# Performance work log

Measured on AMD Instinct MI355X. Metric: run time of the kernel, lower is better.

Reference implementation:

```python
import jax, jax.numpy as jnp
import numpy as np

CHUNK = 32
PRIOR = 64
POSE = 512
PRED = 128
B = 2048


def setup_inputs() -> dict:
    key = jax.random.key(0)
    k1, k2, k3, k4, k5, k6 = jax.random.split(key, 6)
    initial_feature = jax.random.normal(k1, (B, PRIOR, POSE), dtype=jnp.float32)
    pred_feature = jax.random.normal(k2, (B, PRED, POSE), dtype=jnp.float32)
    s1 = 1.0 / np.sqrt(CHUNK * POSE)
    s2 = 1.0 / np.sqrt(POSE)
    W1 = jax.random.uniform(k3, (POSE, CHUNK * POSE), minval=-s1, maxval=s1, dtype=jnp.float32)
    b1 = jax.random.uniform(k4, (POSE,), minval=-s1, maxval=s1, dtype=jnp.float32)
    W2 = jax.random.uniform(k5, (POSE, POSE), minval=-s2, maxval=s2, dtype=jnp.float32)
    b2 = jax.random.uniform(k6, (POSE,), minval=-s2, maxval=s2, dtype=jnp.float32)
    return {"initial_feature": initial_feature, "pred_feature": pred_feature,
            "W1": W1, "b1": b1, "W2": W2, "b2": b2}


def reference(initial_feature, pred_feature, W1, b1, W2, b2):
    Bn = initial_feature.shape[0]
    # last CHUNK prior frames flattened -> [B, CHUNK*POSE]
    x = initial_feature[:, PRIOR - CHUNK:, :].reshape(Bn, -1)
    # spatial_chunk_encoder (Dropout is identity in eval mode)
    mem = (x @ W1.T + b1) @ W2.T + b2          # [B, POSE]
    head = pred_feature[:, :CHUNK, :]          # [B, CHUNK, POSE]
    score = jnp.einsum('bd,bcd->bc', mem, head)  # per-token dot product
    g = jax.nn.sigmoid(score)[..., None]       # [B, CHUNK, 1]
    blended = g * head + (1.0 - g) * mem[:, None, :]
    return pred_feature.at[:, :CHUNK, :].set(blended)
```

## Files before the change

kernel.cpp:

```cpp
#include <hip/hip_runtime.h>
#include <hip/hip_bf16.h>
#include <stdint.h>

#define CHUNKC 32
#define PRIORC 64
#define POSEC 512
#define PREDC 128
#define NB 2048
#define K1 (CHUNKC*POSEC)
#define KS 8
#define KCH (K1/KS)

typedef __attribute__((ext_vector_type(8))) short bf16x8;
typedef __attribute__((ext_vector_type(4))) float f32x4;

__device__ __forceinline__ unsigned short f2b(float f) {
    union { float f; unsigned int u; } x; x.f = f;
    unsigned int r = x.u + 0x7fffu + ((x.u >> 16) & 1u);
    return (unsigned short)(r >> 16);
}

__device__ __forceinline__ void gload_lds16(const void* g, void* l) {
    __builtin_amdgcn_global_load_lds(
        (const __attribute__((address_space(1))) unsigned int*)g,
        (__attribute__((address_space(3))) unsigned int*)l, 16, 0, 0);
}

#define XN4   8388608
#define W1N4  2097152
#define W2N4  65536
__global__ __launch_bounds__(256) void cvt_all_kernel(const float4* __restrict__ init,
                                                      const float4* __restrict__ W1,
                                                      const float4* __restrict__ W2,
                                                      ushort4* __restrict__ xb,
                                                      ushort4* __restrict__ w1b,
                                                      ushort4* __restrict__ w2b) {
    const int64_t n = XN4 + W1N4 + W2N4;
    const int64_t stride = (int64_t)gridDim.x * blockDim.x;
    for (int64_t i = (int64_t)blockIdx.x * blockDim.x + threadIdx.x; i < n; i += stride) {
        float4 v; ushort4* dst;
        if (i < XN4) {
            int64_t b = i >> 12, r = i & 4095;
            v = init[b * 8192 + 4096 + r];
            dst = xb + i;
        } else if (i < XN4 + W1N4) {
            v = W1[i - XN4];
            dst = w1b + (i - XN4);
        } else {
            v = W2[i - XN4 - W1N4];
            dst = w2b + (i - XN4 - W1N4);
        }
        *dst = make_ushort4(f2b(v.x), f2b(v.y), f2b(v.z), f2b(v.w));
    }
}

__global__ __launch_bounds__(256, 4) void gemm1_kernel(const ushort* __restrict__ xb,
                                                       const ushort* __restrict__ w1b,
                                                       float* __restrict__ part) {
    __shared__ ushort As[64][64];
    __shared__ ushort Bs[128][64];
    const int t = threadIdx.x;
    const int l = t & 63, wid = t >> 6;
    const int wr = wid >> 1, wc = wid & 1;
    const int orig = (blockIdx.x & 7) * 128 + (blockIdx.x >> 3);
    const int mt = orig & 31, nt = (orig >> 5) & 3, ks = orig >> 7;

    f32x4 acc[2][4] = {};

    const ushort* aG = xb  + (int64_t)(mt * 64)  * K1 + ks * KCH;
    const ushort* bG = w1b + (int64_t)(nt * 128) * K1 + ks * KCH;
    const int srow = t >> 3, scol = (t & 7) * 8;

    const int fr = l & 15, fq = l >> 4;

    for (int k0 = 0; k0 < KCH; k0 += 64) {
#pragma unroll
        for (int i = 0; i < 2; ++i)
            gload_lds16(aG + (int64_t)(i * 32 + srow) * K1 + k0 + scol,
                        (char*)&As[0][0] + i * 4096 + wid * 1024);
#pragma unroll
        for (int i = 0; i < 4; ++i)
            gload_lds16(bG + (int64_t)(i * 32 + srow) * K1 + k0 + scol,
                        (char*)&Bs[0][0] + i * 4096 + wid * 1024);
        __syncthreads();
#pragma unroll
        for (int k2 = 0; k2 < 2; ++k2) {
            bf16x8 a[2], b[4];
#pragma unroll
            for (int m = 0; m < 2; ++m)
                a[m] = *(const bf16x8*)&As[wr * 32 + m * 16 + fr][k2 * 32 + fq * 8];
#pragma unroll
            for (int n = 0; n < 4; ++n)
                b[n] = *(const bf16x8*)&Bs[wc * 64 + n * 16 + fr][k2 * 32 + fq * 8];
#pragma unroll
            for (int m = 0; m < 2; ++m)
#pragma unroll
                for (int n = 0; n < 4; ++n)
                    acc[m][n] = __builtin_amdgcn_mfma_f32_16x16x32_bf16(a[m], b[n], acc[m][n], 0, 0, 0);
        }
        __syncthreads();
    }

    float* P = part + (int64_t)ks * NB * POSEC;
    const int mbase = mt * 64 + wr * 32, nbase = nt * 128 + wc * 64;
#pragma unroll
    for (int m = 0; m < 2; ++m)
#pragma unroll
        for (int n = 0; n < 4; ++n) {
            int row0 = mbase + m * 16 + fq * 4;
            int col  = nbase + n * 16 + fr;
#pragma unroll
            for (int r = 0; r < 4; ++r)
                P[(int64_t)(row0 + r) * POSEC + col] = acc[m][n][r];
        }
}

__global__ __launch_bounds__(256) void reduce_kernel(const float4* __restrict__ part,
                                                     const float* __restrict__ b1,
                                                     ushort4* __restrict__ A2) {
    const int i4 = blockIdx.x * 256 + threadIdx.x;
    float4 s = part[i4];
#pragma unroll
    for (int k = 1; k < KS; ++k) {
        float4 p = part[(int64_t)k * 262144 + i4];
        s.x += p.x; s.y += p.y; s.z += p.z; s.w += p.w;
    }
    const int col = (i4 * 4) & 511;
    float4 bv = *(const float4*)&b1[col];
    A2[i4] = make_ushort4(f2b(s.x + bv.x), f2b(s.y + bv.y), f2b(s.z + bv.z), f2b(s.w + bv.w));
}

__global__ __launch_bounds__(256) void gemm2_kernel(const ushort* __restrict__ A2,
                                                    const ushort* __restrict__ w2b,
                                                    const float* __restrict__ b2,
                                                    float* __restrict__ mem) {
    __shared__ ushort As[64][64];
    __shared__ ushort Bs[64][64];
    const int t = threadIdx.x;
    const int l = t & 63, wid = t >> 6;
    const int wr = wid >> 1, wc = wid & 1;
    const int mt = blockIdx.x >> 3, nt = blockIdx.x & 7;

    f32x4 acc[2][2] = {};
    const ushort* aG = A2  + (int64_t)(mt * 64) * POSEC;
    const ushort* bG = w2b + (int64_t)(nt * 64) * POSEC;
    const int srow = t >> 3, scol = (t & 7) * 8;
    const int fr = l & 15, fq = l >> 4;

    for (int k0 = 0; k0 < POSEC; k0 += 64) {
#pragma unroll
        for (int i = 0; i < 2; ++i) {
            gload_lds16(aG + (int64_t)(i * 32 + srow) * POSEC + k0 + scol,
                        (char*)&As[0][0] + i * 4096 + wid * 1024);
            gload_lds16(bG + (int64_t)(i * 32 + srow) * POSEC + k0 + scol,
                        (char*)&Bs[0][0] + i * 4096 + wid * 1024);
        }
        __syncthreads();
#pragma unroll
        for (int k2 = 0; k2 < 2; ++k2) {
            bf16x8 a[2], b[2];
#pragma unroll
            for (int m = 0; m < 2; ++m)
                a[m] = *(const bf16x8*)&As[wr * 32 + m * 16 + fr][k2 * 32 + fq * 8];
#pragma unroll
            for (int n = 0; n < 2; ++n)
                b[n] = *(const bf16x8*)&Bs[wc * 32 + n * 16 + fr][k2 * 32 + fq * 8];
#pragma unroll
            for (int m = 0; m < 2; ++m)
#pragma unroll
                for (int n = 0; n < 2; ++n)
                    acc[m][n] = __builtin_amdgcn_mfma_f32_16x16x32_bf16(a[m], b[n], acc[m][n], 0, 0, 0);
        }
        __syncthreads();
    }

    const int mbase = mt * 64 + wr * 32, nbase = nt * 64 + wc * 32;
#pragma unroll
    for (int m = 0; m < 2; ++m)
#pragma unroll
        for (int n = 0; n < 2; ++n) {
            int row0 = mbase + m * 16 + fq * 4;
            int col  = nbase + n * 16 + fr;
            float bias = b2[col];
#pragma unroll
            for (int r = 0; r < 4; ++r)
                mem[(int64_t)(row0 + r) * POSEC + col] = acc[m][n][r] + bias;
        }
}

__global__ __launch_bounds__(256) void blend_kernel(const float* __restrict__ pred,
                                                    const float* __restrict__ mem,
                                                    float* __restrict__ out) {
    const int b = blockIdx.x;
    const int t = threadIdx.x;
    __shared__ float sm[POSEC];
    __shared__ float sg[CHUNKC];

    sm[t]       = mem[(int64_t)b * POSEC + t];
    sm[t + 256] = mem[(int64_t)b * POSEC + 256 + t];
    __syncthreads();

    const int l = t & 63, wid = t >> 6;
    const float4* sm4 = (const float4*)sm;
    const float4* p4 = (const float4*)pred + (int64_t)b * 16384;
    float4* o4 = (float4*)out + (int64_t)b * 16384;

#pragma unroll
    for (int ci = 0; ci < 8; ++ci) {
        int c = wid * 8 + ci;
        float4 h0 = p4[c * 128 + l * 2];
        float4 h1 = p4[c * 128 + l * 2 + 1];
        float4 m0 = sm4[l * 2];
        float4 m1 = sm4[l * 2 + 1];
        float s = h0.x * m0.x + h0.y * m0.y + h0.z * m0.z + h0.w * m0.w
                + h1.x * m1.x + h1.y * m1.y + h1.z * m1.z + h1.w * m1.w;
#pragma unroll
        for (int o = 32; o; o >>= 1) s += __shfl_xor(s, o);
        if (l == 0) sg[c] = 1.0f / (1.0f + expf(-s));
    }
    __syncthreads();

#pragma unroll
    for (int i = 0; i < 16; ++i) {
        int idx = i * 256 + t;
        int row = idx >> 7, c4 = idx & 127;
        float g = sg[row];
        float4 h = p4[idx];
        float4 m = sm4[c4];
        float4 r;
        r.x = g * h.x + (1.0f - g) * m.x;
        r.y = g * h.y + (1.0f - g) * m.y;
        r.z = g * h.z + (1.0f - g) * m.z;
        r.w = g * h.w + (1.0f - g) * m.w;
        o4[idx] = r;
    }
#pragma unroll
    for (int i = 0; i < 48; ++i) {
        int idx = 4096 + i * 256 + t;
        o4[idx] = p4[idx];
    }
}


extern "C" void kernel_launch(void* const* d_in, const int* in_sizes, int n_in,
                              void* d_out, int out_size, void* d_ws, size_t ws_size,
                              hipStream_t stream) {
    const float* init = (const float*)d_in[0];
    const float* pred = (const float*)d_in[1];
    const float* W1   = (const float*)d_in[2];
    const float* b1   = (const float*)d_in[3];
    const float* W2   = (const float*)d_in[4];
    const float* b2   = (const float*)d_in[5];
    float* out = (float*)d_out;

    char* ws = (char*)d_ws;
    ushort* xb   = (ushort*)(ws);
    ushort* w1b  = (ushort*)(ws + 67108864);
    ushort* w2b  = (ushort*)(ws + 83886080);
    float*  part = (float*) (ws + 84410368);
    ushort* A2   = (ushort*)(ws + 117964800);
    float*  mem  = (float*) (ws + 120061952);

    cvt_all_kernel<<<2560, 256, 0, stream>>>((const float4*)init, (const float4*)W1,
                                             (const float4*)W2,
                                             (ushort4*)xb, (ushort4*)w1b, (ushort4*)w2b);
    gemm1_kernel<<<1024, 256, 0, stream>>>(xb, w1b, part);
    reduce_kernel<<<1024, 256, 0, stream>>>((const float4*)part, b1, (ushort4*)A2);
    gemm2_kernel<<<256, 256, 0, stream>>>(A2, w2b, b2, mem);
    blend_kernel<<<NB, 256, 0, stream>>>(pred, mem, out);
}
```

Measured before the change: 345.9 us.

## Enlarge GEMM1 tiles to 256x256 with 512 threads, adaptive split-K, nontemporal copies

GEMM1 moves from 64x128 tiles with 256 threads to 256x256 tiles with 512 threads. Each wave now computes a 128x64 sub-tile (8x4 MFMA fragments), which cuts redundant global and LDS loads of X and W1 per FLOP. Split-K becomes a template parameter: 16 when the workspace is large enough, otherwise 8, so the grid keeps 256 or 128 blocks. The conversion and passthrough copies switch to nontemporal loads and stores to reduce cache pollution. The trade-off is a much larger accumulator register footprint, 64KB of LDS per block and fewer resident blocks, and with KS=8 only 128 blocks, which underfills the GPU.

Result: faster. 333.9 us (-3.5%).

```diff
diff --git a/kernel.cpp b/kernel.cpp
--- a/kernel.cpp
+++ b/kernel.cpp
@@ -8,11 +8,11 @@
 #define PREDC 128
 #define NB 2048
 #define K1 (CHUNKC*POSEC)
-#define KS 8
-#define KCH (K1/KS)
 
 typedef __attribute__((ext_vector_type(8))) short bf16x8;
 typedef __attribute__((ext_vector_type(4))) float f32x4;
+typedef __attribute__((ext_vector_type(4))) float f4v;
+typedef __attribute__((ext_vector_type(4))) unsigned short u16x4;
 
 __device__ __forceinline__ unsigned short f2b(float f) {
     union { float f; unsigned int u; } x; x.f = f;
@@ -29,71 +29,75 @@
 #define XN4   8388608
 #define W1N4  2097152
 #define W2N4  65536
-__global__ __launch_bounds__(256) void cvt_all_kernel(const float4* __restrict__ init,
-                                                      const float4* __restrict__ W1,
-                                                      const float4* __restrict__ W2,
-                                                      ushort4* __restrict__ xb,
-                                                      ushort4* __restrict__ w1b,
-                                                      ushort4* __restrict__ w2b) {
+__global__ __launch_bounds__(256) void cvt_all_kernel(const f4v* __restrict__ init,
+                                                      const f4v* __restrict__ W1,
+                                                      const f4v* __restrict__ W2,
+                                                      u16x4* __restrict__ xb,
+                                                      u16x4* __restrict__ w1b,
+                                                      u16x4* __restrict__ w2b) {
     const int64_t n = XN4 + W1N4 + W2N4;
     const int64_t stride = (int64_t)gridDim.x * blockDim.x;
     for (int64_t i = (int64_t)blockIdx.x * blockDim.x + threadIdx.x; i < n; i += stride) {
-        float4 v; ushort4* dst;
+        f4v v; u16x4* dst;
         if (i < XN4) {
             int64_t b = i >> 12, r = i & 4095;
-            v = init[b * 8192 + 4096 + r];
+            v = __builtin_nontemporal_load(init + b * 8192 + 4096 + r);
             dst = xb + i;
         } else if (i < XN4 + W1N4) {
-            v = W1[i - XN4];
+            v = __builtin_nontemporal_load(W1 + (i - XN4));
             dst = w1b + (i - XN4);
         } else {
-            v = W2[i - XN4 - W1N4];
+            v = __builtin_nontemporal_load(W2 + (i - XN4 - W1N4));
             dst = w2b + (i - XN4 - W1N4);
         }
-        *dst = make_ushort4(f2b(v.x), f2b(v.y), f2b(v.z), f2b(v.w));
-    }
-}
-
-__global__ __launch_bounds__(256, 4) void gemm1_kernel(const ushort* __restrict__ xb,
-                                                       const ushort* __restrict__ w1b,
-                                                       float* __restrict__ part) {
-    __shared__ ushort As[64][64];
-    __shared__ ushort Bs[128][64];
+        u16x4 o;
+        o[0] = f2b(v[0]); o[1] = f2b(v[1]); o[2] = f2b(v[2]); o[3] = f2b(v[3]);
+        __builtin_nontemporal_store(o, dst);
+    }
+}
+
+template<int KSv>
+__global__ __launch_bounds__(512) void gemm1_kernel(const ushort* __restrict__ xb,
+                                                    const ushort* __restrict__ w1b,
+                                                    float* __restrict__ part) {
+    __shared__ ushort As[256][64];
+    __shared__ ushort Bs[256][64];
     const int t = threadIdx.x;
     const int l = t & 63, wid = t >> 6;
-    const int wr = wid >> 1, wc = wid & 1;
-    const int orig = (blockIdx.x & 7) * 128 + (blockIdx.x >> 3);
-    const int mt = orig & 31, nt = (orig >> 5) & 3, ks = orig >> 7;
-
-    f32x4 acc[2][4] = {};
-
-    const ushort* aG = xb  + (int64_t)(mt * 64)  * K1 + ks * KCH;
-    const ushort* bG = w1b + (int64_t)(nt * 128) * K1 + ks * KCH;
+    const int wr = wid >> 2, wc = wid & 3;
+    const int cpx = (16 * KSv) >> 3;
+    const int orig = (blockIdx.x & 7) * cpx + (blockIdx.x >> 3);
+    const int mt = orig & 7, nt = (orig >> 3) & 1, ks = orig >> 4;
+    const int KCHv = K1 / KSv;
+
+    f32x4 acc[8][4] = {};
+
+    const ushort* aG = xb  + (int64_t)(mt * 256) * K1 + ks * KCHv;
+    const ushort* bG = w1b + (int64_t)(nt * 256) * K1 + ks * KCHv;
     const int srow = t >> 3, scol = (t & 7) * 8;
 
     const int fr = l & 15, fq = l >> 4;
 
-    for (int k0 = 0; k0 < KCH; k0 += 64) {
-#pragma unroll
-        for (int i = 0; i < 2; ++i)
-            gload_lds16(aG + (int64_t)(i * 32 + srow) * K1 + k0 + scol,
-                        (char*)&As[0][0] + i * 4096 + wid * 1024);
-#pragma unroll
-        for (int i = 0; i < 4; ++i)
-            gload_lds16(bG + (int64_t)(i * 32 + srow) * K1 + k0 + scol,
-                        (char*)&Bs[0][0] + i * 4096 + wid * 1024);
+    for (int k0 = 0; k0 < KCHv; k0 += 64) {
+#pragma unroll
+        for (int i = 0; i < 4; ++i) {
+            gload_lds16(aG + (int64_t)(i * 64 + srow) * K1 + k0 + scol,
+                        (char*)&As[0][0] + i * 8192 + wid * 1024);
+            gload_lds16(bG + (int64_t)(i * 64 + srow) * K1 + k0 + scol,
+                        (char*)&Bs[0][0] + i * 8192 + wid * 1024);
+        }
         __syncthreads();
 #pragma unroll
         for (int k2 = 0; k2 < 2; ++k2) {
-            bf16x8 a[2], b[4];
-#pragma unroll
-            for (int m = 0; m < 2; ++m)
-                a[m] = *(const bf16x8*)&As[wr * 32 + m * 16 + fr][k2 * 32 + fq * 8];
+            bf16x8 a[8], b[4];
+#pragma unroll
+            for (int m = 0; m < 8; ++m)
+                a[m] = *(const bf16x8*)&As[wr * 128 + m * 16 + fr][k2 * 32 + fq * 8];
 #pragma unroll
             for (int n = 0; n < 4; ++n)
                 b[n] = *(const bf16x8*)&Bs[wc * 64 + n * 16 + fr][k2 * 32 + fq * 8];
 #pragma unroll
-            for (int m = 0; m < 2; ++m)
+            for (int m = 0; m < 8; ++m)
 #pragma unroll
                 for (int n = 0; n < 4; ++n)
                     acc[m][n] = __builtin_amdgcn_mfma_f32_16x16x32_bf16(a[m], b[n], acc[m][n], 0, 0, 0);
@@ -102,9 +106,9 @@
     }
 
     float* P = part + (int64_t)ks * NB * POSEC;
-    const int mbase = mt * 64 + wr * 32, nbase = nt * 128 + wc * 64;
-#pragma unroll
-    for (int m = 0; m < 2; ++m)
+    const int mbase = mt * 256 + wr * 128, nbase = nt * 256 + wc * 64;
+#pragma unroll
+    for (int m = 0; m < 8; ++m)
 #pragma unroll
         for (int n = 0; n < 4; ++n) {
             int row0 = mbase + m * 16 + fq * 4;
@@ -115,13 +119,14 @@
         }
 }
 
+template<int KSv>
 __global__ __launch_bounds__(256) void reduce_kernel(const float4* __restrict__ part,
                                                      const float* __restrict__ b1,
                                                      ushort4* __restrict__ A2) {
     const int i4 = blockIdx.x * 256 + threadIdx.x;
     float4 s = part[i4];
 #pragma unroll
-    for (int k = 1; k < KS; ++k) {
+    for (int k = 1; k < KSv; ++k) {
         float4 p = part[(int64_t)k * 262144 + i4];
         s.x += p.x; s.y += p.y; s.z += p.z; s.w += p.w;
     }
@@ -237,7 +242,8 @@
 #pragma unroll
     for (int i = 0; i < 48; ++i) {
         int idx = 4096 + i * 256 + t;
-        o4[idx] = p4[idx];
+        f4v h = __builtin_nontemporal_load((const f4v*)p4 + idx);
+        __builtin_nontemporal_store(h, (f4v*)o4 + idx);
     }
 }
 
@@ -253,19 +259,27 @@
     const float* b2   = (const float*)d_in[5];
     float* out = (float*)d_out;
 
+    const int KS = (ws_size >= 157810688u) ? 16 : 8;
+
     char* ws = (char*)d_ws;
     ushort* xb   = (ushort*)(ws);
     ushort* w1b  = (ushort*)(ws + 67108864);
     ushort* w2b  = (ushort*)(ws + 83886080);
     float*  part = (float*) (ws + 84410368);
-    ushort* A2   = (ushort*)(ws + 117964800);
-    float*  mem  = (float*) (ws + 120061952);
-
-    cvt_all_kernel<<<2560, 256, 0, stream>>>((const float4*)init, (const float4*)W1,
-                                             (const float4*)W2,
-                                             (ushort4*)xb, (ushort4*)w1b, (ushort4*)w2b);
-    gemm1_kernel<<<1024, 256, 0, stream>>>(xb, w1b, part);
-    reduce_kernel<<<1024, 256, 0, stream>>>((const float4*)part, b1, (ushort4*)A2);
+    char*   after = ws + 84410368 + (size_t)KS * 4194304;
+    ushort* A2   = (ushort*)(after);
+    float*  mem  = (float*) (after + 2097152);
+
+    cvt_all_kernel<<<2560, 256, 0, stream>>>((const f4v*)init, (const f4v*)W1,
+                                             (const f4v*)W2,
+                                             (u16x4*)xb, (u16x4*)w1b, (u16x4*)w2b);
+    if (KS == 16) {
+        gemm1_kernel<16><<<256, 512, 0, stream>>>(xb, w1b, part);
+        reduce_kernel<16><<<1024, 256, 0, stream>>>((const float4*)part, b1, (ushort4*)A2);
+    } else {
+        gemm1_kernel<8><<<128, 512, 0, stream>>>(xb, w1b, part);
+        reduce_kernel<8><<<1024, 256, 0, stream>>>((const float4*)part, b1, (ushort4*)A2);
+    }
     gemm2_kernel<<<256, 256, 0, stream>>>(A2, w2b, b2, mem);
     blend_kernel<<<NB, 256, 0, stream>>>(pred, mem, out);
 }
```
